# Kernel tuning notes

Hardware: AMD Instinct MI355X
Metric: run time of the kernel (lower is better)

The kernel has to match this reference:

```python
import jax, jax.numpy as jnp
import numpy as np

B, C, H, W = 8, 64, 256, 512
FOV = np.pi / 4.0
KH = KW = 3


def _sphere_indices(H, W, fov):
    """Nearest-neighbor gather indices for a 3x3 spherical (gnomonic) kernel
    of angular extent `fov` on an equirectangular grid. Returns int32 [H, W, 9]."""
    taps = [(p, q) for p in (-1, 0, 1) for q in (-1, 0, 1)]
    theta = (0.5 - (np.arange(H) + 0.5) / H) * np.pi            # latitude per row [H]
    phi = ((np.arange(W) + 0.5) / W - 0.5) * 2.0 * np.pi        # longitude per col [W]
    r = np.tan(fov / 2.0)                                       # tangent-plane half extent
    gi_l, gj_l = [], []
    for (p, q) in taps:
        y_t, x_t = p * r, q * r
        rho = np.hypot(x_t, y_t)
        if rho == 0.0:
            lat = theta
            lon_off = np.zeros_like(theta)
        else:
            nu = np.arctan(rho)
            lat = np.arcsin(np.clip(np.cos(nu) * np.sin(theta)
                                    + y_t * np.sin(nu) * np.cos(theta) / rho, -1.0, 1.0))
            lon_off = np.arctan2(x_t * np.sin(nu),
                                 rho * np.cos(theta) * np.cos(nu)
                                 - y_t * np.sin(theta) * np.sin(nu))
        lon = phi[None, :] + lon_off[:, None]                   # [H, W]
        gi = np.clip(np.round((0.5 - lat / np.pi) * H - 0.5), 0, H - 1).astype(np.int32)
        gi = np.broadcast_to(gi[:, None], (H, W)).copy()
        gj = (np.round((lon / (2.0 * np.pi) + 0.5) * W - 0.5).astype(np.int64) % W).astype(np.int32)
        gi_l.append(gi)
        gj_l.append(gj)
    return np.stack(gi_l, axis=-1), np.stack(gj_l, axis=-1)    # [H, W, 9] each


def setup_inputs() -> dict:
    key = jax.random.key(0)
    k1, k2 = jax.random.split(key)
    feature = jax.random.normal(k1, (B, C, H, W), dtype=jnp.float32)
    weight = jax.random.normal(k2, (1, C, KH, KW), dtype=jnp.float32) * 0.05
    gi, gj = _sphere_indices(H, W, FOV)
    return {"feature": feature, "weight": weight,
            "gi": jnp.asarray(gi), "gj": jnp.asarray(gj)}


def reference(feature, weight, gi, gj):
    # SphericalConv: gather-based 3x3 conv over spherical sampling grid, stride 1, no bias.
    O, Cc, kh, kw = weight.shape
    wflat = weight.reshape(O, Cc, kh * kw)                      # [O, C, 9]
    Bb = feature.shape[0]
    Hh, Ww = gi.shape[0], gi.shape[1]
    out = jnp.zeros((Bb, O, Hh, Ww), feature.dtype)
    for k in range(kh * kw):                                    # fixed 9-tap loop
        xk = feature[:, :, gi[:, :, k], gj[:, :, k]]            # gather -> [B, C, H, W]
        out = out + jnp.einsum('bchw,oc->bohw', xk, wflat[:, :, k])
    # nn.Upsample(scale_factor=2) default nearest
    return jnp.repeat(jnp.repeat(out, 2, axis=2), 2, axis=3)
```

## Files before the change

### kernel.cpp

```cpp
#include <hip/hip_runtime.h>

#define Bn   8
#define Cn   64
#define Hn   256
#define Wn   512
#define HWn  (Hn * Wn)
#define TAPS 9

__global__ __launch_bounds__(256) void pass1_chandot(
    const float* __restrict__ feat, const float* __restrict__ wt,
    float* __restrict__ D)
{
    int t   = blockIdx.x * blockDim.x + threadIdx.x;
    int x   = (t & (Wn / 4 - 1)) << 2;
    int row = t >> 7;
    int b   = row >> 8;
    int y   = row & (Hn - 1);

    size_t fbase = (size_t)b * Cn * HWn + (size_t)y * Wn + x;

    float4 acc[TAPS];
#pragma unroll
    for (int k = 0; k < TAPS; ++k) acc[k] = make_float4(0.f, 0.f, 0.f, 0.f);

#pragma unroll 4
    for (int c = 0; c < Cn; ++c) {
        float4 f = *(const float4*)(feat + fbase + (size_t)c * HWn);
#pragma unroll
        for (int k = 0; k < TAPS; ++k) {
            float wv = wt[c * TAPS + k];
            acc[k].x = fmaf(f.x, wv, acc[k].x);
            acc[k].y = fmaf(f.y, wv, acc[k].y);
            acc[k].z = fmaf(f.z, wv, acc[k].z);
            acc[k].w = fmaf(f.w, wv, acc[k].w);
        }
    }

    size_t dbase = (size_t)b * HWn + (size_t)y * Wn + x;
#pragma unroll
    for (int k = 0; k < TAPS; ++k)
        *(float4*)(D + (size_t)k * (Bn * HWn) + dbase) = acc[k];
}

__global__ __launch_bounds__(256) void pass2_gather(
    const float* __restrict__ D, const int* __restrict__ gi,
    const int* __restrict__ gj, float* __restrict__ out)
{
    int p = blockIdx.x * blockDim.x + threadIdx.x;
    int w = p & (Wn - 1);
    int h = (p >> 9) & (Hn - 1);
    int b = p >> 17;

    int iidx = ((h << 9) | w) * TAPS;

    float acc = 0.f;
#pragma unroll
    for (int k = 0; k < TAPS; ++k) {
        int yi = gi[iidx + k];
        int xj = gj[iidx + k];
        acc += D[(size_t)k * (Bn * HWn) + (size_t)b * HWn + yi * Wn + xj];
    }

    float2 v = make_float2(acc, acc);
    size_t o0 = ((size_t)b * (2 * Hn) + 2 * h) * (size_t)(2 * Wn) + 2 * w;
    *(float2*)(out + o0)            = v;
    *(float2*)(out + o0 + 2 * Wn)   = v;
}

__global__ __launch_bounds__(256) void direct_kernel(
    const float* __restrict__ feat, const float* __restrict__ wt,
    const int* __restrict__ gi, const int* __restrict__ gj,
    float* __restrict__ out)
{
    int p = blockIdx.x * blockDim.x + threadIdx.x;
    int w = p & (Wn - 1);
    int h = (p >> 9) & (Hn - 1);
    int b = p >> 17;

    int iidx = ((h << 9) | w) * TAPS;
    int off[TAPS];
#pragma unroll
    for (int k = 0; k < TAPS; ++k)
        off[k] = gi[iidx + k] * Wn + gj[iidx + k];

    float acc = 0.f;
    for (int c = 0; c < Cn; ++c) {
        const float* fc = feat + ((size_t)b * Cn + c) * HWn;
#pragma unroll
        for (int k = 0; k < TAPS; ++k)
            acc = fmaf(fc[off[k]], wt[c * TAPS + k], acc);
    }

    float2 v = make_float2(acc, acc);
    size_t o0 = ((size_t)b * (2 * Hn) + 2 * h) * (size_t)(2 * Wn) + 2 * w;
    *(float2*)(out + o0)          = v;
    *(float2*)(out + o0 + 2 * Wn) = v;
}

extern "C" void kernel_launch(void* const* d_in, const int* in_sizes, int n_in,
                              void* d_out, int out_size, void* d_ws, size_t ws_size,
                              hipStream_t stream) {
    const float* feat = (const float*)d_in[0];
    const float* wt   = (const float*)d_in[1];
    const int*   gi   = (const int*)d_in[2];
    const int*   gj   = (const int*)d_in[3];
    float*       out  = (float*)d_out;

    const size_t needD = (size_t)TAPS * Bn * HWn * sizeof(float);

    if (ws_size >= needD) {
        float* D = (float*)d_ws;
        pass1_chandot<<<(Bn * HWn / 4) / 256, 256, 0, stream>>>(feat, wt, D);
        pass2_gather <<<(Bn * HWn) / 256,     256, 0, stream>>>(D, gi, gj, out);
    } else {
        direct_kernel<<<(Bn * HWn) / 256, 256, 0, stream>>>(feat, wt, gi, gj, out);
    }
}
```

Baseline: 377.2 us.

## Interleave batch in intermediate layout and precompute flat gather offsets

The intermediate tap tensor D changes from [tap][batch][pixel] to [tap][pixel][batch]. Each gather in the second pass now fetches all 8 batches with two float4 loads and reuses one offset across the batch. A new pre-pass flattens gi/gj into a tap-major offset array so the gather reads are coalesced, and the weights are staged in shared memory. The cost is one extra kernel launch, more workspace, 72 accumulators per thread in the channel-dot pass (register pressure), and scalar rather than float4 feature loads in that pass.

```diff
diff --git a/kernel.cpp b/kernel.cpp
--- a/kernel.cpp
+++ b/kernel.cpp
@@ -7,64 +7,83 @@
 #define HWn  (Hn * Wn)
 #define TAPS 9
 
+__global__ __launch_bounds__(256) void pass0_idx(
+    const int* __restrict__ gi, const int* __restrict__ gj,
+    int* __restrict__ off9)
+{
+    int p = blockIdx.x * 256 + threadIdx.x;
+    int base = p * TAPS;
+#pragma unroll
+    for (int k = 0; k < TAPS; ++k)
+        off9[k * HWn + p] = gi[base + k] * Wn + gj[base + k];
+}
+
 __global__ __launch_bounds__(256) void pass1_chandot(
     const float* __restrict__ feat, const float* __restrict__ wt,
     float* __restrict__ D)
 {
-    int t   = blockIdx.x * blockDim.x + threadIdx.x;
-    int x   = (t & (Wn / 4 - 1)) << 2;
-    int row = t >> 7;
-    int b   = row >> 8;
-    int y   = row & (Hn - 1);
+    __shared__ float wl[Cn * TAPS];
+    for (int i = threadIdx.x; i < Cn * TAPS; i += 256) wl[i] = wt[i];
+    __syncthreads();
 
-    size_t fbase = (size_t)b * Cn * HWn + (size_t)y * Wn + x;
+    int p = blockIdx.x * 256 + threadIdx.x;
 
-    float4 acc[TAPS];
+    float acc[TAPS][Bn];
 #pragma unroll
-    for (int k = 0; k < TAPS; ++k) acc[k] = make_float4(0.f, 0.f, 0.f, 0.f);
+    for (int k = 0; k < TAPS; ++k)
+#pragma unroll
+        for (int b = 0; b < Bn; ++b) acc[k][b] = 0.f;
 
-#pragma unroll 4
+#pragma unroll 2
     for (int c = 0; c < Cn; ++c) {
-        float4 f = *(const float4*)(feat + fbase + (size_t)c * HWn);
+        float f[Bn];
+#pragma unroll
+        for (int b = 0; b < Bn; ++b)
+            f[b] = feat[((size_t)b * Cn + c) * HWn + p];
 #pragma unroll
         for (int k = 0; k < TAPS; ++k) {
-            float wv = wt[c * TAPS + k];
-            acc[k].x = fmaf(f.x, wv, acc[k].x);
-            acc[k].y = fmaf(f.y, wv, acc[k].y);
-            acc[k].z = fmaf(f.z, wv, acc[k].z);
-            acc[k].w = fmaf(f.w, wv, acc[k].w);
+            float wv = wl[c * TAPS + k];
+#pragma unroll
+            for (int b = 0; b < Bn; ++b)
+                acc[k][b] = fmaf(f[b], wv, acc[k][b]);
         }
     }
 
-    size_t dbase = (size_t)b * HWn + (size_t)y * Wn + x;
 #pragma unroll
-    for (int k = 0; k < TAPS; ++k)
-        *(float4*)(D + (size_t)k * (Bn * HWn) + dbase) = acc[k];
+    for (int k = 0; k < TAPS; ++k) {
+        float4* dst = (float4*)(D + ((size_t)k * HWn + p) * Bn);
+        dst[0] = make_float4(acc[k][0], acc[k][1], acc[k][2], acc[k][3]);
+        dst[1] = make_float4(acc[k][4], acc[k][5], acc[k][6], acc[k][7]);
+    }
 }
 
 __global__ __launch_bounds__(256) void pass2_gather(
-    const float* __restrict__ D, const int* __restrict__ gi,
-    const int* __restrict__ gj, float* __restrict__ out)
+    const float* __restrict__ D, const int* __restrict__ off9,
+    float* __restrict__ out)
 {
-    int p = blockIdx.x * blockDim.x + threadIdx.x;
+    int p = blockIdx.x * 256 + threadIdx.x;
     int w = p & (Wn - 1);
-    int h = (p >> 9) & (Hn - 1);
-    int b = p >> 17;
+    int h = p >> 9;
 
-    int iidx = ((h << 9) | w) * TAPS;
-
-    float acc = 0.f;
+    float4 a0 = make_float4(0.f, 0.f, 0.f, 0.f);
+    float4 a1 = make_float4(0.f, 0.f, 0.f, 0.f);
 #pragma unroll
     for (int k = 0; k < TAPS; ++k) {
-        int yi = gi[iidx + k];
-        int xj = gj[iidx + k];
-        acc += D[(size_t)k * (Bn * HWn) + (size_t)b * HWn + yi * Wn + xj];
+        int off = off9[k * HWn + p];
+        const float4* d = (const float4*)(D + ((size_t)k * HWn + off) * Bn);
+        float4 d0 = d[0], d1 = d[1];
+        a0.x += d0.x; a0.y += d0.y; a0.z += d0.z; a0.w += d0.w;
+        a1.x += d1.x; a1.y += d1.y; a1.z += d1.z; a1.w += d1.w;
     }
 
-    float2 v = make_float2(acc, acc);
-    size_t o0 = ((size_t)b * (2 * Hn) + 2 * h) * (size_t)(2 * Wn) + 2 * w;
-    *(float2*)(out + o0)            = v;
-    *(float2*)(out + o0 + 2 * Wn)   = v;
+    float vals[Bn] = {a0.x, a0.y, a0.z, a0.w, a1.x, a1.y, a1.z, a1.w};
+#pragma unroll
+    for (int b = 0; b < Bn; ++b) {
+        float2 vv = make_float2(vals[b], vals[b]);
+        size_t o = ((size_t)b * (2 * Hn) + 2 * h) * (size_t)(2 * Wn) + 2 * w;
+        *(float2*)(out + o)            = vv;
+        *(float2*)(out + o + 2 * Wn)   = vv;
+    }
 }
 
 __global__ __launch_bounds__(256) void direct_kernel(
@@ -106,12 +125,15 @@
     const int*   gj   = (const int*)d_in[3];
     float*       out  = (float*)d_out;
 
-    const size_t needD = (size_t)TAPS * Bn * HWn * sizeof(float);
+    const size_t bytesD   = (size_t)TAPS * HWn * Bn * sizeof(float);
+    const size_t bytesOff = (size_t)TAPS * HWn * sizeof(int);
 
-    if (ws_size >= needD) {
-        float* D = (float*)d_ws;
-        pass1_chandot<<<(Bn * HWn / 4) / 256, 256, 0, stream>>>(feat, wt, D);
-        pass2_gather <<<(Bn * HWn) / 256,     256, 0, stream>>>(D, gi, gj, out);
+    if (ws_size >= bytesD + bytesOff) {
+        float* D    = (float*)d_ws;
+        int*   off9 = (int*)((char*)d_ws + bytesD);
+        pass0_idx    <<<HWn / 256, 256, 0, stream>>>(gi, gj, off9);
+        pass1_chandot<<<HWn / 256, 256, 0, stream>>>(feat, wt, D);
+        pass2_gather <<<HWn / 256, 256, 0, stream>>>(D, off9, out);
     } else {
         direct_kernel<<<(Bn * HWn) / 256, 256, 0, stream>>>(feat, wt, gi, gj, out);
     }
```

After: 406.0 us. 7.6% more time.
